# Kernel optimization log

Hardware: AMD Instinct MI355X
Metric: run time of the kernel (lower is better)

## Reference

```python
import jax, jax.numpy as jnp
import numpy as np

N, P, C, IMG = 65536, 2048, 3, 256


def setup_inputs() -> dict:
    key = jax.random.key(0)
    k1, k2, k3, k4 = jax.random.split(key, 4)
    X = jax.random.randint(k1, (N, 2), 0, IMG, dtype=jnp.int32)
    pattern_layer = jax.random.randint(k2, (P, 2), 0, IMG, dtype=jnp.int32)
    W2 = jax.random.normal(k3, (C, P), dtype=jnp.float32)
    # sigma >= 1 per module docstring; adapt_sigma yields per-node values
    sigmaSq = jax.random.uniform(k4, (P,), dtype=jnp.float32) * 4.0 + 1.0
    return {"X": X, "pattern_layer": pattern_layer, "W2": W2, "sigmaSq": sigmaSq}


def reference(X, pattern_layer, W2, sigmaSq):
    # Squared L2 distance from each query pixel to each pattern node, [N, P].
    # Coords are small ints, so the expanded form is exact in fp32.
    Xf = X.astype(jnp.float32)
    Pf = pattern_layer.astype(jnp.float32)
    Dsq = ((Xf * Xf).sum(-1)[:, None]
           + (Pf * Pf).sum(-1)[None, :]
           - 2.0 * Xf @ Pf.T)
    # Gaussian RBF with per-node bandwidth sigmaSq, [N, P]
    rbf = jnp.exp(-Dsq / (2.0 * sigmaSq))
    den = rbf.sum(axis=1)                       # [N]
    num = jnp.einsum('np,cp->nc', rbf, W2)      # [N, C]
    return num / den[:, None]
```

## Files before the change

### kernel.cpp

```cpp
#include <hip/hip_runtime.h>
#include <math.h>

#ifndef __has_builtin
#define __has_builtin(x) 0
#endif

#define GRIDC  32
#define NCELL  1024
#define CSHIFT 3
#define RAD    4

__device__ __forceinline__ float fast_exp2(float x) {
#if __has_builtin(__builtin_amdgcn_exp2f)
    return __builtin_amdgcn_exp2f(x);
#else
    return exp2f(x);
#endif
}

__device__ __forceinline__ int cell_of(int x, int y) {
    int cx = x >> CSHIFT; cx = cx < 0 ? 0 : (cx > GRIDC - 1 ? GRIDC - 1 : cx);
    int cy = y >> CSHIFT; cy = cy < 0 ? 0 : (cy > GRIDC - 1 ? GRIDC - 1 : cy);
    return (cy << 5) + cx;
}

__global__ __launch_bounds__(512) void rbf_fused(const int* __restrict__ X,
        const int* __restrict__ pat, const float* __restrict__ W2,
        const float* __restrict__ sig, float* __restrict__ out, int N, int P) {
    __shared__ float4 sA[2048];
    __shared__ float2 sB[2048];
    __shared__ int    sst[NCELL + 1];
    __shared__ float4 accb[3 * 128];
    __shared__ int    wsum[8];

    const int tid  = threadIdx.x;
    const int lane = tid & 63;
    const int wv   = tid >> 6;

    for (int i = tid; i < NCELL + 1; i += 512) sst[i] = 0;
    __syncthreads();

    int cellr[4], slotr[4], xr[4], yr[4];
#pragma unroll
    for (int j = 0; j < 4; ++j) {
        int p = j * 512 + tid;
        cellr[j] = -1;
        if (p < P) {
            int2 xy = ((const int2*)pat)[p];
            xr[j] = xy.x; yr[j] = xy.y;
            int c = cell_of(xy.x, xy.y);
            cellr[j] = c;
            slotr[j] = atomicAdd(&sst[c], 1);
        }
    }
    __syncthreads();

    const int c0 = sst[2 * tid], c1 = sst[2 * tid + 1];
    int sum = c0 + c1;
    int incl = sum;
#pragma unroll
    for (int off = 1; off < 64; off <<= 1) {
        int t = __shfl_up(incl, off);
        if (lane >= off) incl += t;
    }
    if (lane == 63) wsum[wv] = incl;
    __syncthreads();
    int base = 0;
#pragma unroll
    for (int w = 0; w < 8; ++w) base += (w < wv) ? wsum[w] : 0;
    const int excl0 = base + incl - sum;
    __syncthreads();
    sst[2 * tid + 0] = excl0;
    sst[2 * tid + 1] = excl0 + c0;
    if (tid == 511) sst[NCELL] = excl0 + c0 + c1;
    __syncthreads();

#pragma unroll
    for (int j = 0; j < 4; ++j) {
        if (cellr[j] >= 0) {
            int p = j * 512 + tid;
            int pos = sst[cellr[j]] + slotr[j];
            sA[pos] = make_float4((float)xr[j], (float)yr[j],
                                  -0.7213475204444817f / sig[p], W2[p]);
            sB[pos] = make_float2(W2[P + p], W2[2 * P + p]);
        }
    }
    __syncthreads();

    const int quarter = tid >> 7;
    const int qi      = tid & 127;
    const int n       = blockIdx.x * 128 + qi;
    const bool act    = n < N;

    float den = 0.f, acc0 = 0.f, acc1 = 0.f, acc2 = 0.f;
    if (act) {
        int2 xy = ((const int2*)X)[n];
        const float xf = (float)xy.x, yf = (float)xy.y;
        int cx = xy.x >> CSHIFT; cx = cx < 0 ? 0 : (cx > GRIDC - 1 ? GRIDC - 1 : cx);
        int cy = xy.y >> CSHIFT; cy = cy < 0 ? 0 : (cy > GRIDC - 1 ? GRIDC - 1 : cy);
        const int x0 = cx - RAD < 0 ? 0 : cx - RAD;
        const int x1 = cx + RAD > GRIDC - 1 ? GRIDC - 1 : cx + RAD;
        const int r0 = (9 * quarter) >> 2;
        const int r1 = (9 * (quarter + 1)) >> 2;
        for (int r = r0; r < r1; ++r) {
            int gy = cy - RAD + r;
            if ((unsigned)gy >= GRIDC) continue;
            int row = gy << 5;
            int k0 = sst[row + x0];
            int k1 = sst[row + x1 + 1];
            if (k0 >= k1) continue;
            float4 a = sA[k0];
            float2 b = sB[k0];
            for (int k = k0; k < k1; ++k) {
                int kn = k + 1 < k1 ? k + 1 : k;
                float4 an = sA[kn];
                float2 bn = sB[kn];
                float dx = xf - a.x;
                float dy = yf - a.y;
                float rr = fast_exp2(fmaf(dy, dy, dx * dx) * a.z);
                den  += rr;
                acc0 = fmaf(rr, a.w, acc0);
                acc1 = fmaf(rr, b.x, acc1);
                acc2 = fmaf(rr, b.y, acc2);
                a = an; b = bn;
            }
        }
    }

    if (quarter) accb[(quarter - 1) * 128 + qi] = make_float4(den, acc0, acc1, acc2);
    __syncthreads();
    if (quarter == 0 && act) {
#pragma unroll
        for (int w = 0; w < 3; ++w) {
            float4 u = accb[w * 128 + qi];
            den += u.x; acc0 += u.y; acc1 += u.z; acc2 += u.w;
        }
        float inv = 1.0f / den;
        out[3 * n + 0] = acc0 * inv;
        out[3 * n + 1] = acc1 * inv;
        out[3 * n + 2] = acc2 * inv;
    }
}

__global__ void pack_nodes(const int* __restrict__ pat, const float* __restrict__ W2,
                           const float* __restrict__ sigmaSq, float* __restrict__ nodes,
                           int P) {
    int p = blockIdx.x * blockDim.x + threadIdx.x;
    if (p >= P) return;
    float* q = nodes + 8 * (size_t)p;
    q[0] = (float)pat[2 * p];
    q[1] = (float)pat[2 * p + 1];
    q[2] = -0.7213475204444817f / sigmaSq[p];
    q[3] = W2[p];
    q[4] = W2[P + p];
    q[5] = W2[2 * P + p];
    q[6] = 0.0f;
    q[7] = 0.0f;
}

__global__ __launch_bounds__(256) void rbf_main_dyn(const int* __restrict__ X,
                                                    const float* __restrict__ nodes,
                                                    float* __restrict__ outp,
                                                    int N, int P) {
    int n = blockIdx.x * 256 + threadIdx.x;
    if (n >= N) return;
    float xn = (float)X[2 * n], yn = (float)X[2 * n + 1];
    float den = 0.f, a0 = 0.f, a1 = 0.f, a2 = 0.f;
    for (int j = 0; j < P; ++j) {
        const float* q = nodes + (size_t)j * 8;
        float dx = xn - q[0], dy = yn - q[1];
        float r = fast_exp2(fmaf(dy, dy, dx * dx) * q[2]);
        den += r;
        a0 = fmaf(r, q[3], a0);
        a1 = fmaf(r, q[4], a1);
        a2 = fmaf(r, q[5], a2);
    }
    outp[3 * n + 0] = a0 / den;
    outp[3 * n + 1] = a1 / den;
    outp[3 * n + 2] = a2 / den;
}

extern "C" void kernel_launch(void* const* d_in, const int* in_sizes, int n_in,
                              void* d_out, int out_size, void* d_ws, size_t ws_size,
                              hipStream_t stream) {
    const int*   X   = (const int*)d_in[0];
    const int*   pat = (const int*)d_in[1];
    const float* W2  = (const float*)d_in[2];
    const float* sig = (const float*)d_in[3];
    float*       out = (float*)d_out;

    const int N = in_sizes[0] / 2;
    const int P = in_sizes[3];

    if (P <= 2048 && out_size == 3 * N) {
        rbf_fused<<<dim3((N + 127) / 128), dim3(512), 0, stream>>>(
            X, pat, W2, sig, out, N, P);
    } else {
        float* nodes = (float*)d_ws;
        pack_nodes<<<dim3((P + 255) / 256), dim3(256), 0, stream>>>(pat, W2, sig, nodes, P);
        rbf_main_dyn<<<dim3((N + 255) / 256), dim3(256), 0, stream>>>(X, nodes, out, N, P);
    }
}
```

Baseline: 72.34 us.

## Counting-sort queries by grid cell and split node loops across lanes

Adds a histogram pass and a scatter pass that bucket query pixels by spatial grid cell, so each wavefront handles spatially adjacent queries with similar neighbour-cell ranges. The main kernel then processes 16 queries per wave, with 4 lanes per query striding through the node list and combining partial sums via shuffles. This targets the lane divergence caused by random query positions having different neighbour counts. In exchange it costs two extra kernel launches, a memset and workspace traffic.

```diff
diff --git a/kernel.cpp b/kernel.cpp
--- a/kernel.cpp
+++ b/kernel.cpp
@@ -22,6 +22,167 @@
     int cx = x >> CSHIFT; cx = cx < 0 ? 0 : (cx > GRIDC - 1 ? GRIDC - 1 : cx);
     int cy = y >> CSHIFT; cy = cy < 0 ? 0 : (cy > GRIDC - 1 ? GRIDC - 1 : cy);
     return (cy << 5) + cx;
+}
+
+__global__ __launch_bounds__(256) void qhist_k(const int* __restrict__ X,
+        int* __restrict__ qcount, int* __restrict__ qslot, int N) {
+    int n = blockIdx.x * 256 + threadIdx.x;
+    if (n >= N) return;
+    int2 xy = ((const int2*)X)[n];
+    qslot[n] = atomicAdd(&qcount[cell_of(xy.x, xy.y)], 1);
+}
+
+__global__ __launch_bounds__(256) void qscatter_k(const int* __restrict__ X,
+        const int* __restrict__ qcount, const int* __restrict__ qslot,
+        int* __restrict__ qidx, int N) {
+    __shared__ int qstart[NCELL];
+    __shared__ int wsum4[4];
+    const int tid = threadIdx.x;
+    const int lane = tid & 63;
+    const int wv = tid >> 6;
+    int c0 = qcount[4 * tid + 0], c1 = qcount[4 * tid + 1];
+    int c2 = qcount[4 * tid + 2], c3 = qcount[4 * tid + 3];
+    int sum = c0 + c1 + c2 + c3;
+    int incl = sum;
+#pragma unroll
+    for (int off = 1; off < 64; off <<= 1) {
+        int t = __shfl_up(incl, off);
+        if (lane >= off) incl += t;
+    }
+    if (lane == 63) wsum4[wv] = incl;
+    __syncthreads();
+    int base = 0;
+#pragma unroll
+    for (int w = 0; w < 4; ++w) base += (w < wv) ? wsum4[w] : 0;
+    const int e = base + incl - sum;
+    qstart[4 * tid + 0] = e;
+    qstart[4 * tid + 1] = e + c0;
+    qstart[4 * tid + 2] = e + c0 + c1;
+    qstart[4 * tid + 3] = e + c0 + c1 + c2;
+    __syncthreads();
+    int n = blockIdx.x * 256 + tid;
+    if (n < N) {
+        int2 xy = ((const int2*)X)[n];
+        int c = cell_of(xy.x, xy.y);
+        qidx[qstart[c] + qslot[n]] = n;
+    }
+}
+
+__global__ __launch_bounds__(512) void rbf_sorted(const int* __restrict__ X,
+        const int* __restrict__ pat, const float* __restrict__ W2,
+        const float* __restrict__ sig, const int* __restrict__ qidx,
+        float* __restrict__ out, int N, int P) {
+    __shared__ float4 sA[2048];
+    __shared__ float2 sB[2048];
+    __shared__ int    sst[NCELL + 1];
+    __shared__ int    wsum[8];
+
+    const int tid  = threadIdx.x;
+    const int lane = tid & 63;
+    const int wv   = tid >> 6;
+
+    for (int i = tid; i < NCELL + 1; i += 512) sst[i] = 0;
+    __syncthreads();
+
+    int cellr[4], slotr[4], xr[4], yr[4];
+#pragma unroll
+    for (int j = 0; j < 4; ++j) {
+        int p = j * 512 + tid;
+        cellr[j] = -1;
+        if (p < P) {
+            int2 xy = ((const int2*)pat)[p];
+            xr[j] = xy.x; yr[j] = xy.y;
+            int c = cell_of(xy.x, xy.y);
+            cellr[j] = c;
+            slotr[j] = atomicAdd(&sst[c], 1);
+        }
+    }
+    __syncthreads();
+
+    const int c0 = sst[2 * tid], c1 = sst[2 * tid + 1];
+    int sum = c0 + c1;
+    int incl = sum;
+#pragma unroll
+    for (int off = 1; off < 64; off <<= 1) {
+        int t = __shfl_up(incl, off);
+        if (lane >= off) incl += t;
+    }
+    if (lane == 63) wsum[wv] = incl;
+    __syncthreads();
+    int base = 0;
+#pragma unroll
+    for (int w = 0; w < 8; ++w) base += (w < wv) ? wsum[w] : 0;
+    const int excl0 = base + incl - sum;
+    __syncthreads();
+    sst[2 * tid + 0] = excl0;
+    sst[2 * tid + 1] = excl0 + c0;
+    if (tid == 511) sst[NCELL] = excl0 + c0 + c1;
+    __syncthreads();
+
+#pragma unroll
+    for (int j = 0; j < 4; ++j) {
+        if (cellr[j] >= 0) {
+            int p = j * 512 + tid;
+            int pos = sst[cellr[j]] + slotr[j];
+            sA[pos] = make_float4((float)xr[j], (float)yr[j],
+                                  -0.7213475204444817f / sig[p], W2[p]);
+            sB[pos] = make_float2(W2[P + p], W2[2 * P + p]);
+        }
+    }
+    __syncthreads();
+
+    const int h  = lane >> 4;
+    const int qs = lane & 15;
+    const int j  = blockIdx.x * 128 + wv * 16 + qs;
+    const bool act = j < N;
+
+    float den = 0.f, acc0 = 0.f, acc1 = 0.f, acc2 = 0.f;
+    int n0 = 0;
+    if (act) {
+        n0 = qidx[j];
+        int2 xy = ((const int2*)X)[n0];
+        const float xf = (float)xy.x, yf = (float)xy.y;
+        int cx = xy.x >> CSHIFT; cx = cx < 0 ? 0 : (cx > GRIDC - 1 ? GRIDC - 1 : cx);
+        int cy = xy.y >> CSHIFT; cy = cy < 0 ? 0 : (cy > GRIDC - 1 ? GRIDC - 1 : cy);
+        const int x0 = cx - RAD < 0 ? 0 : cx - RAD;
+        const int x1 = cx + RAD > GRIDC - 1 ? GRIDC - 1 : cx + RAD;
+        const int y0 = cy - RAD < 0 ? 0 : cy - RAD;
+        const int y1 = cy + RAD > GRIDC - 1 ? GRIDC - 1 : cy + RAD;
+        for (int gy = y0; gy <= y1; ++gy) {
+            int row = gy << 5;
+            int k0 = sst[row + x0];
+            int k1 = sst[row + x1 + 1];
+            int k = k0 + h;
+            if (k >= k1) continue;
+            float4 a = sA[k];
+            float2 b = sB[k];
+            for (; k < k1; k += 4) {
+                int kn = k + 4 < k1 ? k + 4 : k;
+                float4 an = sA[kn];
+                float2 bn = sB[kn];
+                float dx = xf - a.x;
+                float dy = yf - a.y;
+                float rr = fast_exp2(fmaf(dy, dy, dx * dx) * a.z);
+                den  += rr;
+                acc0 = fmaf(rr, a.w, acc0);
+                acc1 = fmaf(rr, b.x, acc1);
+                acc2 = fmaf(rr, b.y, acc2);
+                a = an; b = bn;
+            }
+        }
+    }
+
+    den  += __shfl_xor(den,  16); acc0 += __shfl_xor(acc0, 16);
+    acc1 += __shfl_xor(acc1, 16); acc2 += __shfl_xor(acc2, 16);
+    den  += __shfl_xor(den,  32); acc0 += __shfl_xor(acc0, 32);
+    acc1 += __shfl_xor(acc1, 32); acc2 += __shfl_xor(acc2, 32);
+
+    if (act && h == 0) {
+        float inv = 1.0f / den;
+        out[3 * n0 + 0] = acc0 * inv;
+        out[3 * n0 + 1] = acc1 * inv;
+        out[3 * n0 + 2] = acc2 * inv;
+    }
 }
 
 __global__ __launch_bounds__(512) void rbf_fused(const int* __restrict__ X,
@@ -193,8 +354,20 @@
     const int P = in_sizes[3];
 
     if (P <= 2048 && out_size == 3 * N) {
-        rbf_fused<<<dim3((N + 127) / 128), dim3(512), 0, stream>>>(
-            X, pat, W2, sig, out, N, P);
+        const size_t need = (size_t)(NCELL + 2 * (size_t)N) * sizeof(int);
+        if (ws_size >= need && N >= 4096) {
+            int* qcount = (int*)d_ws;
+            int* qslot  = qcount + NCELL;
+            int* qidx   = qslot + N;
+            hipMemsetAsync(qcount, 0, NCELL * sizeof(int), stream);
+            qhist_k<<<dim3((N + 255) / 256), dim3(256), 0, stream>>>(X, qcount, qslot, N);
+            qscatter_k<<<dim3((N + 255) / 256), dim3(256), 0, stream>>>(X, qcount, qslot, qidx, N);
+            rbf_sorted<<<dim3((N + 127) / 128), dim3(512), 0, stream>>>(
+                X, pat, W2, sig, qidx, out, N, P);
+        } else {
+            rbf_fused<<<dim3((N + 127) / 128), dim3(512), 0, stream>>>(
+                X, pat, W2, sig, out, N, P);
+        }
     } else {
         float* nodes = (float*)d_ws;
         pack_nodes<<<dim3((P + 255) / 256), dim3(256), 0, stream>>>(pat, W2, sig, nodes, P);
```

Result: slower. 88.46 us (+22.3%).
